# Kernel optimization log

Hardware: AMD Instinct MI355X
Metric: run time of the kernel (lower is better)

The kernel has to match this reference:

```python
import jax, jax.numpy as jnp
import numpy as np
from jax import lax

SCALE = 2
NUM_POINTS = 4

def conv2d(x, w, b, pad):
    # x: [B,C,H,W], w: [O,I,kh,kw]
    y = lax.conv_general_dilated(x, w, (1, 1), [(pad, pad), (pad, pad)],
                                 dimension_numbers=("NCHW", "OIHW", "NCHW"))
    return y + b[None, :, None, None]

def grid_sample_border(feat, grid):
    # feat: [B,C,H,W]; grid: [B,Hg,Wg,2] in [-1,1] (x,y), align_corners=False,
    # padding_mode='border' (coordinates clipped before interpolation, as in torch).
    B, C, H, W = feat.shape
    Hg, Wg = grid.shape[1], grid.shape[2]
    gx = jnp.clip((grid[..., 0] + 1.0) * W / 2.0 - 0.5, 0.0, W - 1.0)
    gy = jnp.clip((grid[..., 1] + 1.0) * H / 2.0 - 0.5, 0.0, H - 1.0)
    x0 = jnp.floor(gx); y0 = jnp.floor(gy)
    fx = (gx - x0).reshape(B, 1, -1)
    fy = (gy - y0).reshape(B, 1, -1)
    x0i = jnp.clip(x0.astype(jnp.int32), 0, W - 1)
    y0i = jnp.clip(y0.astype(jnp.int32), 0, H - 1)
    x1i = jnp.clip(x0i + 1, 0, W - 1)
    y1i = jnp.clip(y0i + 1, 0, H - 1)
    featf = feat.reshape(B, C, H * W)
    def gather(yi, xi):
        idx = (yi * W + xi).reshape(B, 1, -1)
        return jnp.take_along_axis(featf, idx, axis=2)  # [B,C,Hg*Wg]
    v00 = gather(y0i, x0i); v01 = gather(y0i, x1i)
    v10 = gather(y1i, x0i); v11 = gather(y1i, x1i)
    out = (v00 * (1 - fx) * (1 - fy) + v01 * fx * (1 - fy)
           + v10 * (1 - fx) * fy + v11 * fx * fy)
    return out.reshape(B, C, Hg, Wg)

def setup_inputs() -> dict:
    key = jax.random.key(0)
    ks = jax.random.split(key, 8)
    B, Cin, Cout, H, W = 8, 256, 256, 64, 64
    high_feat = jax.random.normal(ks[0], (B, Cin, H, W), jnp.float32)
    low_feat = jax.random.normal(ks[1], (B, Cout, H * SCALE, W * SCALE), jnp.float32)
    W1 = jax.random.normal(ks[2], (Cin, Cin + Cout, 1, 1), jnp.float32) * 0.02
    b1 = jnp.zeros((Cin,), jnp.float32)
    # original inits offset_conv2 to zeros; use small random to exercise deformable sampling
    W2 = jax.random.normal(ks[3], (NUM_POINTS * 2, Cin, 3, 3), jnp.float32) * 0.01
    b2 = jnp.zeros((NUM_POINTS * 2,), jnp.float32)
    Wf = jax.random.normal(ks[4], (Cout, Cin, 1, 1), jnp.float32) * 0.05
    bf = jnp.zeros((Cout,), jnp.float32)
    return {"high_feat": high_feat, "low_feat": low_feat, "W1": W1, "b1": b1,
            "W2": W2, "b2": b2, "Wf": Wf, "bf": bf}

def reference(high_feat, low_feat, W1, b1, W2, b2, Wf, bf):
    B, Cin, H, W = high_feat.shape
    H_up, W_up = H * SCALE, W * SCALE
    # bilinear upsample, align_corners=False (half-pixel centers)
    up_high = jax.image.resize(high_feat, (B, Cin, H_up, W_up), method="bilinear")
    concat = jnp.concatenate([up_high, low_feat], axis=1)
    off_feat = jax.nn.relu(conv2d(concat, W1, b1, 0))
    offsets = conv2d(off_feat, W2, b2, 1)  # [B, 2P, H_up, W_up]
    proc = conv2d(high_feat, Wf, bf, 0)    # [B, Cout, H, W]
    # base grid in [-1,1], (x,y)
    gy = jnp.linspace(-1.0, 1.0, H_up)
    gx = jnp.linspace(-1.0, 1.0, W_up)
    base = jnp.stack(jnp.meshgrid(gx, gy, indexing="xy"), axis=-1)  # [H_up,W_up,2]
    # offsets -> [B,P,2,H,W] -> [P,B,H,W,2], normalized to [-1,1] units
    off = offsets.reshape(B, NUM_POINTS, 2, H_up, W_up).transpose(1, 0, 3, 4, 2)
    norm = jnp.array([W_up, H_up], jnp.float32)
    off = off / norm * 2.0
    grids = base[None, None] + off  # [P,B,H_up,W_up,2]
    sampled = jax.vmap(lambda g: grid_sample_border(proc, g))(grids)  # [P,B,C,H_up,W_up]
    return jnp.mean(sampled, axis=0)
```

## Files before the change

### kernel.cpp

```cpp
#include <hip/hip_runtime.h>
#include <stdint.h>

#define NB   8
#define CH   256
#define HW0  4096
#define HW2  16384

typedef __attribute__((ext_vector_type(8))) short short8;
typedef __attribute__((ext_vector_type(8))) unsigned short u16x8;
typedef __attribute__((ext_vector_type(4))) unsigned short u16x4;
typedef __attribute__((ext_vector_type(4))) float floatx4;

__device__ inline unsigned short f2bf(float f) {
    union { float f; uint32_t u; } v; v.f = f;
    return (unsigned short)((v.u + 0x7FFFu + ((v.u >> 16) & 1u)) >> 16);
}
__device__ inline float bf2f(unsigned short h) {
    union { uint32_t u; float f; } v; v.u = ((uint32_t)h) << 16;
    return v.f;
}

__global__ __launch_bounds__(256) void ktrans(const float* __restrict__ src,
        unsigned short* __restrict__ dst, int M) {
    const int b = blockIdx.z, k0 = blockIdx.y * 32, m0 = blockIdx.x * 128;
    const int tid = threadIdx.x;
    __shared__ unsigned short tile[32][132];
    const float* s = src + ((size_t)b * CH + k0) * M + m0;
    for (int c = tid; c < 1024; c += 256) {
        int kk = c >> 5, mm = (c & 31) * 4;
        float4 v = *(const float4*)(s + (size_t)kk * M + mm);
        u16x4 o = { f2bf(v.x), f2bf(v.y), f2bf(v.z), f2bf(v.w) };
        *(u16x4*)&tile[kk][mm] = o;
    }
    __syncthreads();
    unsigned short* d = dst + ((size_t)b * M + m0) * CH + k0;
    for (int c = tid; c < 512; c += 256) {
        int mm = c >> 2, kc = (c & 3) * 8;
        u16x8 v;
        #pragma unroll
        for (int i = 0; i < 8; ++i) v[i] = tile[kc + i][mm];
        *(u16x8*)(d + (size_t)mm * CH + kc) = v;
    }
}

__global__ __launch_bounds__(256) void kwconv(const float* __restrict__ W1,
        const float* __restrict__ Wf, unsigned short* __restrict__ A1,
        unsigned short* __restrict__ A2) {
    int i = blockIdx.x * 256 + threadIdx.x;
    if (i < 512 * 256) {
        int n = i >> 8, k = i & 255;
        float v = (n < 256) ? W1[n * 512 + k] : Wf[(size_t)(n - 256) * 256 + k];
        A1[i] = f2bf(v);
    }
    if (i < 256 * 256) {
        int n = i >> 8, k = i & 255;
        A2[i] = f2bf(W1[n * 512 + 256 + k]);
    }
}

__global__ __launch_bounds__(256) void kwpack(const float* __restrict__ W2v,
        unsigned short* __restrict__ W3p) {
    int i = blockIdx.x * 256 + threadIdx.x;
    if (i >= 9 * 16 * 256) return;
    int ci = i & 255, o = (i >> 8) & 15, t = i >> 12;
    float v = (o < 8) ? W2v[((size_t)o * 256 + ci) * 9 + t] : 0.0f;
    W3p[i] = f2bf(v);
}

__global__ __launch_bounds__(256) void k1_mfma(
    const unsigned short* __restrict__ highT,
    const unsigned short* __restrict__ A1,
    const float* __restrict__ bfv,
    float* __restrict__ T, float* __restrict__ procT)
{
    const int bid = blockIdx.x;
    const int b  = bid & 7;
    const int q  = bid >> 3;
    const int m0 = (q & 31) * 128;
    const int n0 = (q >> 5) * 128;
    const int tid = threadIdx.x;
    __shared__ __attribute__((aligned(16))) unsigned short smem[2 * 128 * 40];
    unsigned short* As = smem;
    unsigned short* Xs = smem + 128 * 40;
    const int lane = tid & 63, wid = tid >> 6;
    const int wn = (wid >> 1) * 64, wm = (wid & 1) * 64;
    const int l15 = lane & 15, quad = lane >> 4;

    floatx4 acc[4][4];
    #pragma unroll
    for (int i = 0; i < 4; ++i)
        #pragma unroll
        for (int j = 0; j < 4; ++j)
            acc[i][j] = (floatx4){0.f, 0.f, 0.f, 0.f};

    const unsigned short* Xg = highT + ((size_t)b * HW0 + m0) * CH;

    for (int k0 = 0; k0 < 256; k0 += 32) {
        for (int c = tid; c < 512; c += 256) {
            int row = c >> 2, kc = (c & 3) * 8;
            *(u16x8*)&As[row * 40 + kc] =
                *(const u16x8*)(A1 + (size_t)(n0 + row) * CH + k0 + kc);
            *(u16x8*)&Xs[row * 40 + kc] =
                *(const u16x8*)(Xg + (size_t)row * CH + k0 + kc);
        }
        __syncthreads();
        short8 af[4], bfr[4];
        #pragma unroll
        for (int i = 0; i < 4; ++i)
            af[i] = *(const short8*)&As[(wn + i * 16 + l15) * 40 + quad * 8];
        #pragma unroll
        for (int j = 0; j < 4; ++j)
            bfr[j] = *(const short8*)&Xs[(wm + j * 16 + l15) * 40 + quad * 8];
        #pragma unroll
        for (int i = 0; i < 4; ++i)
            #pragma unroll
            for (int j = 0; j < 4; ++j)
                acc[i][j] = __builtin_amdgcn_mfma_f32_16x16x32_bf16(
                    af[i], bfr[j], acc[i][j], 0, 0, 0);
        __syncthreads();
    }

    if (n0 < 256) {
        #pragma unroll
        for (int i = 0; i < 4; ++i) {
            int nb = n0 + wn + i * 16 + quad * 4;
            #pragma unroll
            for (int r = 0; r < 4; ++r) {
                int n = nb + r;
                #pragma unroll
                for (int j = 0; j < 4; ++j) {
                    int m = m0 + wm + j * 16 + l15;
                    T[((size_t)b * CH + n) * HW0 + m] = acc[i][j][r];
                }
            }
        }
    } else {
        float* tf = (float*)smem;
        const int nc = n0 - 256;
        #pragma unroll
        for (int mq = 0; mq < 4; ++mq) {
            __syncthreads();
            if ((wid & 1) == (mq >> 1)) {
                #pragma unroll
                for (int jj = 0; jj < 2; ++jj) {
                    int j = (mq & 1) * 2 + jj;
                    int ml = j * 16 + l15 - (mq & 1) * 32;
                    #pragma unroll
                    for (int i = 0; i < 4; ++i) {
                        int nl = wn + i * 16 + quad * 4;
                        #pragma unroll
                        for (int r = 0; r < 4; ++r)
                            tf[ml * 132 + nl + r] = acc[i][j][r] + bfv[nc + nl + r];
                    }
                }
            }
            __syncthreads();
            int mm = tid >> 3;
            int c8 = tid & 7;
            float* dst = procT + ((size_t)b * HW0 + m0 + mq * 32 + mm) * CH + nc;
            #pragma unroll
            for (int k = 0; k < 4; ++k) {
                int col = c8 * 4 + k * 32;
                *(float4*)(dst + col) = *(const float4*)&tf[mm * 132 + col];
            }
        }
    }
}

__global__ __launch_bounds__(256) void k2_mfma(
    const float* __restrict__ low,
    const unsigned short* __restrict__ A2,
    const float* __restrict__ b1, const float* __restrict__ T,
    unsigned short* __restrict__ off_featT)
{
    const int bid = blockIdx.x;
    const int b  = bid & 7;
    const int q  = bid >> 3;
    const int y  = q >> 1;
    const int n0 = (q & 1) * 128;
    const int tid = threadIdx.x;
    __shared__ unsigned short smem[2 * 128 * 40];
    unsigned short* As = smem;
    unsigned short* Xs = smem + 128 * 40;
    const int lane = tid & 63, wid = tid >> 6;
    const int wn = (wid >> 1) * 64, wm = (wid & 1) * 64;
    const int l15 = lane & 15, quad = lane >> 4;

    const int rowA = lane + (wid & 1) * 64;
    const int slA  = wid >> 1;
    const float* Lg = low + ((size_t)b * CH + wid * 8) * HW2
                      + (size_t)y * 128 + lane;

    floatx4 acc[4][4];
    #pragma unroll
    for (int i = 0; i < 4; ++i)
        #pragma unroll
        for (int j = 0; j < 4; ++j)
            acc[i][j] = (floatx4){0.f, 0.f, 0.f, 0.f};

    u16x8 aR[2];
    float xR[2][8];

    #pragma unroll
    for (int i = 0; i < 2; ++i)
        aR[i] = *(const u16x8*)(A2 + (size_t)(n0 + rowA) * CH + (slA + i * 2) * 8);
    #pragma unroll
    for (int i = 0; i < 2; ++i)
        #pragma unroll
        for (int c = 0; c < 8; ++c)
            xR[i][c] = Lg[(size_t)c * HW2 + i * 64];

    for (int k0 = 0; k0 < 256; k0 += 32) {
        __syncthreads();
        #pragma unroll
        for (int i = 0; i < 2; ++i)
            *(u16x8*)&As[rowA * 40 + (slA + i * 2) * 8] = aR[i];
        #pragma unroll
        for (int i = 0; i < 2; ++i) {
            u16x8 o = { f2bf(xR[i][0]), f2bf(xR[i][1]), f2bf(xR[i][2]),
                        f2bf(xR[i][3]), f2bf(xR[i][4]), f2bf(xR[i][5]),
                        f2bf(xR[i][6]), f2bf(xR[i][7]) };
            *(u16x8*)&Xs[(lane + i * 64) * 40 + wid * 8] = o;
        }
        __syncthreads();
        if (k0 + 32 < 256) {
            #pragma unroll
            for (int i = 0; i < 2; ++i)
                aR[i] = *(const u16x8*)(A2 + (size_t)(n0 + rowA) * CH
                                        + k0 + 32 + (slA + i * 2) * 8);
            #pragma unroll
            for (int i = 0; i < 2; ++i)
                #pragma unroll
                for (int c = 0; c < 8; ++c)
                    xR[i][c] = Lg[(size_t)(k0 + 32 + c) * HW2 + i * 64];
        }
        short8 af[4], bfr[4];
        #pragma unroll
        for (int i = 0; i < 4; ++i)
            af[i] = *(const short8*)&As[(wn + i * 16 + l15) * 40 + quad * 8];
        #pragma unroll
        for (int j = 0; j < 4; ++j)
            bfr[j] = *(const short8*)&Xs[(wm + j * 16 + l15) * 40 + quad * 8];
        #pragma unroll
        for (int i = 0; i < 4; ++i)
            #pragma unroll
            for (int j = 0; j < 4; ++j)
                acc[i][j] = __builtin_amdgcn_mfma_f32_16x16x32_bf16(
                    af[i], bfr[j], acc[i][j], 0, 0, 0);
    }

    int hk = y >> 1;
    int yA, yB; float wyA, wyB;
    if (y & 1) { yA = hk; yB = min(hk + 1, 63); wyA = 0.75f; wyB = 0.25f; }
    else       { yB = hk; yA = max(hk - 1, 0);  wyA = 0.25f; wyB = 0.75f; }

    int xA[4], xB[4]; float wxA[4], wxB[4];
    #pragma unroll
    for (int j = 0; j < 4; ++j) {
        int x = wm + j * 16 + l15;
        int xk = x >> 1;
        if (x & 1) { xA[j] = xk; xB[j] = min(xk + 1, 63); wxA[j] = 0.75f; wxB[j] = 0.25f; }
        else       { xB[j] = xk; xA[j] = max(xk - 1, 0);  wxA[j] = 0.25f; wxB[j] = 0.75f; }
    }

    #pragma unroll
    for (int i = 0; i < 4; ++i) {
        int nb = n0 + wn + i * 16 + quad * 4;
        #pragma unroll
        for (int r = 0; r < 4; ++r) {
            int n = nb + r;
            const float* tb  = T + ((size_t)b * CH + n) * HW0;
            const float* trA = tb + yA * 64;
            const float* trB = tb + yB * 64;
            float bias = b1[n];
            #pragma unroll
            for (int j = 0; j < 4; ++j) {
                float up = wyA * (wxA[j] * trA[xA[j]] + wxB[j] * trA[xB[j]])
                         + wyB * (wxA[j] * trB[xA[j]] + wxB[j] * trB[xB[j]]);
                acc[i][j][r] = fmaxf(acc[i][j][r] + up + bias, 0.0f);
            }
        }
    }

    unsigned short (*tile)[136] = (unsigned short (*)[136])smem;
    for (int xh = 0; xh < 2; ++xh) {
        __syncthreads();
        if ((wid & 1) == xh) {
            #pragma unroll
            for (int i = 0; i < 4; ++i) {
                int nc = wn + i * 16 + quad * 4;
                #pragma unroll
                for (int j = 0; j < 4; ++j) {
                    int xr = j * 16 + l15;
                    unsigned int lo = (unsigned int)f2bf(acc[i][j][0])
                                    | ((unsigned int)f2bf(acc[i][j][1]) << 16);
                    unsigned int hi = (unsigned int)f2bf(acc[i][j][2])
                                    | ((unsigned int)f2bf(acc[i][j][3]) << 16);
                    *(unsigned int*)&tile[xr][nc]     = lo;
                    *(unsigned int*)&tile[xr][nc + 2] = hi;
                }
            }
        }
        __syncthreads();
        for (int c = tid; c < 1024; c += 256) {
            int xr = c >> 4, nc = (c & 15) * 8;
            u16x8 v = *(u16x8*)&tile[xr][nc];
            *(u16x8*)(off_featT +
                ((size_t)b * HW2 + (size_t)y * 128 + xh * 64 + xr) * CH + n0 + nc) = v;
        }
    }
}

__global__ __launch_bounds__(256) void k3_mfma(
    const unsigned short* __restrict__ offT,
    const unsigned short* __restrict__ W3p,
    float* __restrict__ offs)
{
    const int bid = blockIdx.x;
    const int b  = bid & 7;
    const int q  = bid >> 3;
    const int y  = q >> 2;
    const int xq = q & 3;
    const int tid = threadIdx.x;
    const int lane = tid & 63, w = tid >> 6;
    const int l15 = lane & 15, quad = lane >> 4;

    __shared__ __attribute__((aligned(16))) unsigned short st[3 * 34 * 256];

    short8 bw[9][2];
    #pragma unroll
    for (int t = 0; t < 9; ++t)
        #pragma unroll
        for (int k0 = 0; k0 < 2; ++k0)
            bw[t][k0] = *(const short8*)(W3p + (size_t)(t * 16 + l15) * CH
                                         + w * 64 + k0 * 32 + quad * 8);

    const unsigned short* src = offT + (size_t)b * HW2 * CH;
    for (int it = tid; it < 3264; it += 256) {
        int s   = it & 31;
        int px  = (it >> 5) % 34;
        int row = it / (34 * 32);
        int gy = y - 1 + row;
        int gx = xq * 32 - 1 + px;
        u16x8 v = (u16x8){0, 0, 0, 0, 0, 0, 0, 0};
        if ((unsigned)gy < 128u && (unsigned)gx < 128u)
            v = *(const u16x8*)(src + ((size_t)gy * 128 + gx) * CH + s * 8);
        *(u16x8*)&st[(row * 34 + px) * 256 + ((s ^ (px & 7)) * 8)] = v;
    }
    __syncthreads();

    floatx4 acc[2];
    acc[0] = (floatx4){0.f, 0.f, 0.f, 0.f};
    acc[1] = (floatx4){0.f, 0.f, 0.f, 0.f};

    #pragma unroll
    for (int k0 = 0; k0 < 2; ++k0) {
        #pragma unroll
        for (int t = 0; t < 9; ++t) {
            const int row = t / 3, dxi = t % 3;
            const int srd = w * 8 + k0 * 4 + quad;
            #pragma unroll
            for (int j = 0; j < 2; ++j) {
                int px = j * 16 + l15 + dxi;
                short8 a = *(const short8*)&st[(row * 34 + px) * 256
                                               + ((srd ^ (px & 7)) * 8)];
                acc[j] = __builtin_amdgcn_mfma_f32_16x16x32_bf16(
                    a, bw[t][k0], acc[j], 0, 0, 0);
            }
        }
    }

    __syncthreads();
    float* red = (float*)st;
    #pragma unroll
    for (int j = 0; j < 2; ++j)
        #pragma unroll
        for (int r = 0; r < 4; ++r)
            red[(w * 32 + j * 16 + quad * 4 + r) * 16 + l15] = acc[j][r];
    __syncthreads();

    const int oc = tid >> 5, px = tid & 31;
    float s0 = red[px * 16 + oc]        + red[(32 + px) * 16 + oc]
             + red[(64 + px) * 16 + oc] + red[(96 + px) * 16 + oc];
    offs[((size_t)b * 8 + oc) * HW2 + (size_t)y * 128 + xq * 32 + px] = s0;
}

__global__ __launch_bounds__(256) void k4_sample(
    const float* __restrict__ offs, const float* __restrict__ b2v,
    const float* __restrict__ procT, float* __restrict__ out)
{
    const int blk = blockIdx.x;
    const int b  = blk & 7;
    const int r  = blk >> 3;
    const int y  = r >> 1;
    const int xh = r & 1;
    const int tid = threadIdx.x;
    const int lane = tid & 63, w = tid >> 6;

    __shared__ int2   sp_i[4][64];
    __shared__ float4 sp_w[4][64];
    __shared__ float  tile[4][8 * 260];

    if (tid < 64) {
        int x = xh * 64 + tid;
        float gxb = (2.0f * x) / 127.0f - 1.0f;
        float gyb = (2.0f * y) / 127.0f - 1.0f;
        const float* ob = offs + (size_t)b * 8 * HW2 + y * 128 + x;
        #pragma unroll
        for (int p = 0; p < 4; ++p) {
            float ox = ob[(2 * p) * HW2] + b2v[2 * p];
            float oy = ob[(2 * p + 1) * HW2] + b2v[2 * p + 1];
            float gx = gxb + ox * (2.0f / 128.0f);
            float gy = gyb + oy * (2.0f / 128.0f);
            float gxp = fminf(fmaxf((gx + 1.0f) * 32.0f - 0.5f, 0.0f), 63.0f);
            float gyp = fminf(fmaxf((gy + 1.0f) * 32.0f - 0.5f, 0.0f), 63.0f);
            float x0f = floorf(gxp), y0f = floorf(gyp);
            int x0 = (int)x0f, y0 = (int)y0f;
            int idx = (y0 * 64 + x0) * 256;
            int dxo = (x0 < 63) ? 256 : 0;
            int dyo = (y0 < 63) ? 16384 : 0;
            float fx = gxp - x0f, fy = gyp - y0f;
            float ex = 1.0f - fx, ey = 1.0f - fy;
            sp_i[p][tid] = make_int2(idx, dxo | (dyo << 16));
            sp_w[p][tid] = make_float4(0.25f * ex * ey, 0.25f * fx * ey,
                                       0.25f * ex * fy, 0.25f * fx * fy);
        }
    }
    __syncthreads();

    const float* P = procT + (size_t)b * HW0 * CH + lane * 4;
    float* tw = &tile[w][0];
    float* outb = out + (size_t)b * CH * HW2 + (size_t)y * 128 + xh * 64 + w * 16;

    for (int c8 = 0; c8 < 2; ++c8) {
        #pragma unroll
        for (int i = 0; i < 8; ++i) {
            int lpx = w * 16 + c8 * 8 + i;
            float4 a = make_float4(0.f, 0.f, 0.f, 0.f);
            #pragma unroll
            for (int p = 0; p < 4; ++p) {
                int2 si = sp_i[p][lpx];
                float4 sw = sp_w[p][lpx];
                int dxo = si.y & 0xFFFF, dyo = si.y >> 16;
                const float* qp = P + si.x;
                float4 v00 = *(const float4*)(qp);
                float4 v01 = *(const float4*)(qp + dxo);
                float4 v10 = *(const float4*)(qp + dyo);
                float4 v11 = *(const float4*)(qp + dyo + dxo);
                a.x += sw.x * v00.x + sw.y * v01.x + sw.z * v10.x + sw.w * v11.x;
                a.y += sw.x * v00.y + sw.y * v01.y + sw.z * v10.y + sw.w * v11.y;
                a.z += sw.x * v00.z + sw.y * v01.z + sw.z * v10.z + sw.w * v11.z;
                a.w += sw.x * v00.w + sw.y * v01.w + sw.z * v10.w + sw.w * v11.w;
            }
            *(float4*)&tw[i * 260 + lane * 4] = a;
        }
        __syncthreads();
        #pragma unroll
        for (int g = 0; g < 32; ++g) {
            int c   = g * 8 + (lane >> 3);
            int pxl = lane & 7;
            outb[(size_t)c * HW2 + c8 * 8 + pxl] = tw[pxl * 260 + c];
        }
        __syncthreads();
    }
}

extern "C" void kernel_launch(void* const* d_in, const int* in_sizes, int n_in,
                              void* d_out, int out_size, void* d_ws, size_t ws_size,
                              hipStream_t stream) {
    const float* high = (const float*)d_in[0];
    const float* low  = (const float*)d_in[1];
    const float* W1   = (const float*)d_in[2];
    const float* b1   = (const float*)d_in[3];
    const float* W2v  = (const float*)d_in[4];
    const float* b2v  = (const float*)d_in[5];
    const float* Wf   = (const float*)d_in[6];
    const float* bfv  = (const float*)d_in[7];
    float* out = (float*)d_out;
    float* ws  = (float*)d_ws;

    float* T     = ws;
    float* procT = ws + 8388608;
    float* offs  = ws + 16777216;
    unsigned short* highT = (unsigned short*)(ws + 17825792);
    unsigned short* A1 = highT + 8388608;
    unsigned short* A2 = A1 + 131072;

    unsigned short* W3p = highT;

    unsigned short* off_featT = ((unsigned short*)out) + 33554432;

    ktrans<<<dim3(32, 8, NB), 256, 0, stream>>>(high, highT, HW0);
    kwconv<<<dim3(512), 256, 0, stream>>>(W1, Wf, A1, A2);

    k1_mfma<<<dim3(1024), 256, 0, stream>>>(highT, A1, bfv, T, procT);
    kwpack<<<dim3(144), 256, 0, stream>>>(W2v, W3p);
    k2_mfma<<<dim3(2048), 256, 0, stream>>>(low, A2, b1, T, off_featT);
    k3_mfma<<<dim3(4096), 256, 0, stream>>>(off_featT, W3p, offs);
    k4_sample<<<dim3(2048), 256, 0, stream>>>(offs, b2v, procT, out);
}
```

Measured before the change: 503.6 us.

## Shrink sampler LDS footprint and raise occupancy in deformable sample kernel

The sampling kernel now stores each sample point as a packed int (index plus two border flags) and a float2 of fractional coords instead of int2 plus float4 weights. The bilinear weights are recomputed per use and the 0.25 mean factor is applied once at the end. The transpose tile shrinks from 8 to 4 pixels per pass, with padding 264, and launch bounds request 8 blocks per CU. The aim is to cut LDS and register use so more waves can hide gather latency. In exchange, the output stores become shorter per channel row (4 contiguous floats instead of 8) and there are twice as many barrier-separated passes.

```diff
diff --git a/kernel.cpp b/kernel.cpp
--- a/kernel.cpp
+++ b/kernel.cpp
@@ -385,7 +385,7 @@
     offs[((size_t)b * 8 + oc) * HW2 + (size_t)y * 128 + xq * 32 + px] = s0;
 }
 
-__global__ __launch_bounds__(256) void k4_sample(
+__global__ __launch_bounds__(256, 8) void k4_sample(
     const float* __restrict__ offs, const float* __restrict__ b2v,
     const float* __restrict__ procT, float* __restrict__ out)
 {
@@ -397,9 +397,9 @@
     const int tid = threadIdx.x;
     const int lane = tid & 63, w = tid >> 6;
 
-    __shared__ int2   sp_i[4][64];
-    __shared__ float4 sp_w[4][64];
-    __shared__ float  tile[4][8 * 260];
+    __shared__ int    sp_i[4][64];
+    __shared__ float2 sp_f[4][64];
+    __shared__ float  tile[4][4 * 264];
 
     if (tid < 64) {
         int x = xh * 64 + tid;
@@ -417,13 +417,9 @@
             float x0f = floorf(gxp), y0f = floorf(gyp);
             int x0 = (int)x0f, y0 = (int)y0f;
             int idx = (y0 * 64 + x0) * 256;
-            int dxo = (x0 < 63) ? 256 : 0;
-            int dyo = (y0 < 63) ? 16384 : 0;
-            float fx = gxp - x0f, fy = gyp - y0f;
-            float ex = 1.0f - fx, ey = 1.0f - fy;
-            sp_i[p][tid] = make_int2(idx, dxo | (dyo << 16));
-            sp_w[p][tid] = make_float4(0.25f * ex * ey, 0.25f * fx * ey,
-                                       0.25f * ex * fy, 0.25f * fx * fy);
+            int fl  = ((x0 < 63) ? (1 << 20) : 0) | ((y0 < 63) ? (1 << 21) : 0);
+            sp_i[p][tid] = idx | fl;
+            sp_f[p][tid] = make_float2(gxp - x0f, gyp - y0f);
         }
     }
     __syncthreads();
@@ -432,34 +428,40 @@
     float* tw = &tile[w][0];
     float* outb = out + (size_t)b * CH * HW2 + (size_t)y * 128 + xh * 64 + w * 16;
 
-    for (int c8 = 0; c8 < 2; ++c8) {
-        #pragma unroll
-        for (int i = 0; i < 8; ++i) {
-            int lpx = w * 16 + c8 * 8 + i;
+    for (int c4 = 0; c4 < 4; ++c4) {
+        #pragma unroll
+        for (int i = 0; i < 4; ++i) {
+            int lpx = w * 16 + c4 * 4 + i;
             float4 a = make_float4(0.f, 0.f, 0.f, 0.f);
             #pragma unroll
             for (int p = 0; p < 4; ++p) {
-                int2 si = sp_i[p][lpx];
-                float4 sw = sp_w[p][lpx];
-                int dxo = si.y & 0xFFFF, dyo = si.y >> 16;
-                const float* qp = P + si.x;
+                int si = sp_i[p][lpx];
+                float2 f = sp_f[p][lpx];
+                int idx = si & 0xFFFFF;
+                int dxo = (si & (1 << 20)) ? 256 : 0;
+                int dyo = (si & (1 << 21)) ? 16384 : 0;
+                float fx = f.x, fy = f.y;
+                float ex = 1.0f - fx, ey = 1.0f - fy;
+                float w00 = ex * ey, w01 = fx * ey, w10 = ex * fy, w11 = fx * fy;
+                const float* qp = P + idx;
                 float4 v00 = *(const float4*)(qp);
                 float4 v01 = *(const float4*)(qp + dxo);
                 float4 v10 = *(const float4*)(qp + dyo);
                 float4 v11 = *(const float4*)(qp + dyo + dxo);
-                a.x += sw.x * v00.x + sw.y * v01.x + sw.z * v10.x + sw.w * v11.x;
-                a.y += sw.x * v00.y + sw.y * v01.y + sw.z * v10.y + sw.w * v11.y;
-                a.z += sw.x * v00.z + sw.y * v01.z + sw.z * v10.z + sw.w * v11.z;
-                a.w += sw.x * v00.w + sw.y * v01.w + sw.z * v10.w + sw.w * v11.w;
-            }
-            *(float4*)&tw[i * 260 + lane * 4] = a;
-        }
-        __syncthreads();
-        #pragma unroll
-        for (int g = 0; g < 32; ++g) {
-            int c   = g * 8 + (lane >> 3);
-            int pxl = lane & 7;
-            outb[(size_t)c * HW2 + c8 * 8 + pxl] = tw[pxl * 260 + c];
+                a.x += w00 * v00.x + w01 * v01.x + w10 * v10.x + w11 * v11.x;
+                a.y += w00 * v00.y + w01 * v01.y + w10 * v10.y + w11 * v11.y;
+                a.z += w00 * v00.z + w01 * v01.z + w10 * v10.z + w11 * v11.z;
+                a.w += w00 * v00.w + w01 * v01.w + w10 * v10.w + w11 * v11.w;
+            }
+            a.x *= 0.25f; a.y *= 0.25f; a.z *= 0.25f; a.w *= 0.25f;
+            *(float4*)&tw[i * 264 + lane * 4] = a;
+        }
+        __syncthreads();
+        #pragma unroll
+        for (int g = 0; g < 16; ++g) {
+            int c   = g * 16 + (lane >> 2);
+            int pxl = lane & 3;
+            outb[(size_t)c * HW2 + c4 * 4 + pxl] = tw[pxl * 264 + c];
         }
         __syncthreads();
     }
```

Measured after the change: 810.2 us. 60.9% more time.
